# Kernel optimization log

Measured on AMD Instinct MI355X. Metric: run time of the kernel, lower is better.

## Reference

```python
import jax, jax.numpy as jnp
import numpy as np

N_VERT = 40962  # icosphere level-6 vertex count
K = 7           # 1-ring neighborhood size (self + 6 neighbors)


def setup_inputs() -> dict:
    key = jax.random.key(0)
    k1, k2, k3 = jax.random.split(key, 3)
    x = jax.random.normal(k1, (16, 256, N_VERT), dtype=jnp.float32)
    neigh_orders = jax.random.randint(k2, (N_VERT * K,), 0, N_VERT, dtype=jnp.int32)
    W = jax.random.normal(k3, (1, 2 * K), dtype=jnp.float32) * 0.1  # Linear(14 -> 1) weight
    b = jnp.zeros((1,), dtype=jnp.float32)
    return {"x": x, "neigh_orders": neigh_orders, "W": W, "b": b}


def reference(x, neigh_orders, W, b):
    # x: [B, C, N] features on spherical mesh vertices
    avg = jnp.mean(x, axis=1, keepdims=True)          # [B, 1, N] (AdaptiveAvgPool2d((1,None)))
    mx = jnp.max(x, axis=1, keepdims=True)            # [B, 1, N] (AdaptiveMaxPool2d((1,None)))
    pool = jnp.concatenate([avg, mx], axis=1)         # [B, 2, N]
    p = jnp.transpose(pool, (0, 2, 1))                # [B, N, 2]
    idx = neigh_orders.reshape(N_VERT, K)             # [N, 7] 1-ring neighbor indices
    g = p[:, idx, :]                                  # [B, N, 7, 2] neighbor gather
    g = g.reshape(p.shape[0], N_VERT, 2 * K)          # [B, N, 14]
    out = jnp.einsum('bnf,of->bno', g, W) + b         # [B, N, 1] Linear(14 -> 1)
    att = jax.nn.sigmoid(out)
    return jnp.transpose(att, (0, 2, 1))              # [B, 1, N] spatial attention map
```

## Files before the change

### kernel.cpp

```cpp
#include <hip/hip_runtime.h>
#include <math.h>

#define B_DIM 16
#define C_DIM 256
#define NV    40962
#define K_NEI 7
#define GRP   10240
#define MAIN_BLOCKS 2560

typedef float v2f __attribute__((ext_vector_type(2)));

__global__ __launch_bounds__(64) void pool_kernel(const float* __restrict__ x,
                                                  float4* __restrict__ pool) {
    if (blockIdx.x < MAIN_BLOCKS) {
        int t  = blockIdx.x * 64 + threadIdx.x;
        int b  = t / GRP;
        int r  = t - b * GRP;
        int n0 = 4 * r;

        const float* xb = x + (size_t)b * C_DIM * NV + n0;

        float s0 = 0.f, s1 = 0.f, s2 = 0.f, s3 = 0.f;
        float m0 = -INFINITY, m1 = -INFINITY, m2 = -INFINITY, m3 = -INFINITY;
        #pragma unroll 16
        for (int c = 0; c < C_DIM; ++c) {
            const float* p = xb + (size_t)c * NV;
            v2f va = __builtin_nontemporal_load(reinterpret_cast<const v2f*>(p));
            v2f vb = __builtin_nontemporal_load(reinterpret_cast<const v2f*>(p + 2));
            s0 += va.x; s1 += va.y; s2 += vb.x; s3 += vb.y;
            m0 = fmaxf(m0, va.x); m1 = fmaxf(m1, va.y);
            m2 = fmaxf(m2, vb.x); m3 = fmaxf(m3, vb.y);
        }
        const float inv = 1.0f / (float)C_DIM;
        size_t f4 = ((size_t)b * NV + n0) >> 1;
        pool[f4]     = make_float4(s0 * inv, m0, s1 * inv, m1);
        pool[f4 + 1] = make_float4(s2 * inv, m2, s3 * inv, m3);
    } else {
        __shared__ float2 part[64];
        int tid  = threadIdx.x;
        int col  = tid >> 1;
        int half = tid & 1;
        int b    = col >> 1;
        int n    = 40960 + (col & 1);

        const float* xb = x + (size_t)b * C_DIM * NV + n;
        float s = 0.f, m = -INFINITY;
        #pragma unroll 8
        for (int c = half * 128; c < half * 128 + 128; ++c) {
            float v = xb[(size_t)c * NV];
            s += v; m = fmaxf(m, v);
        }
        part[tid] = make_float2(s, m);
        __syncthreads();
        if (half == 0) {
            float2 a = part[tid], bb2 = part[tid + 1];
            float2* poolf2 = reinterpret_cast<float2*>(pool);
            poolf2[(size_t)b * NV + n] =
                make_float2((a.x + bb2.x) * (1.0f / (float)C_DIM), fmaxf(a.y, bb2.y));
        }
    }
}

__global__ void transpose_kernel(const float2* __restrict__ pool,
                                 float2* __restrict__ poolT) {
    __shared__ float2 tile[64][17];
    int n0 = blockIdx.x * 64;
    int i  = threadIdx.x & 63;
    int bq = threadIdx.x >> 6;
    #pragma unroll
    for (int p = 0; p < 4; ++p) {
        int b = p * 4 + bq;
        if (n0 + i < NV)
            tile[i][b] = pool[(size_t)b * NV + n0 + i];
    }
    __syncthreads();
    int valid = NV - n0; if (valid > 64) valid = 64;
    int nf4 = valid * 8;
    float4* dst = reinterpret_cast<float4*>(poolT + (size_t)n0 * 16);
    for (int e = threadIdx.x; e < nf4; e += 256) {
        int e2 = e * 2;
        int n  = e2 >> 4;
        int b  = e2 & 15;
        float2 a0 = tile[n][b];
        float2 a1 = tile[n][b + 1];
        dst[e] = make_float4(a0.x, a0.y, a1.x, a1.y);
    }
}

__global__ void att4_kernel(const float2* __restrict__ poolT,
                            const int* __restrict__ idx,
                            const float* __restrict__ W,
                            const float* __restrict__ bias,
                            float* __restrict__ out) {
    int tid = threadIdx.x;
    int n   = blockIdx.x * 64 + (tid >> 2);
    int bq  = tid & 3;
    if (n >= NV) return;

    float w[2 * K_NEI];
    #pragma unroll
    for (int i = 0; i < 2 * K_NEI; ++i) w[i] = W[i];
    float bb = bias[0];

    float acc[4];
    #pragma unroll
    for (int r = 0; r < 4; ++r) acc[r] = bb;

    #pragma unroll
    for (int k = 0; k < K_NEI; ++k) {
        int j = idx[n * K_NEI + k];
        const float4* L = reinterpret_cast<const float4*>(poolT + (size_t)j * 16 + bq * 4);
        float4 v0 = L[0];
        float4 v1 = L[1];
        acc[0] = fmaf(w[2 * k + 1], v0.y, fmaf(w[2 * k], v0.x, acc[0]));
        acc[1] = fmaf(w[2 * k + 1], v0.w, fmaf(w[2 * k], v0.z, acc[1]));
        acc[2] = fmaf(w[2 * k + 1], v1.y, fmaf(w[2 * k], v1.x, acc[2]));
        acc[3] = fmaf(w[2 * k + 1], v1.w, fmaf(w[2 * k], v1.z, acc[3]));
    }
    #pragma unroll
    for (int r = 0; r < 4; ++r)
        out[(size_t)(bq * 4 + r) * NV + n] = 1.0f / (1.0f + expf(-acc[r]));
}

extern "C" void kernel_launch(void* const* d_in, const int* in_sizes, int n_in,
                              void* d_out, int out_size, void* d_ws, size_t ws_size,
                              hipStream_t stream) {
    const float* x     = (const float*)d_in[0];
    const int*   neigh = (const int*)  d_in[1];
    const float* W     = (const float*)d_in[2];
    const float* bias  = (const float*)d_in[3];
    float*       out   = (float*)d_out;

    const size_t POOL_BYTES = (size_t)B_DIM * NV * sizeof(float2);

    float4* pool4 = (float4*)d_ws;
    float2* poolT = (float2*)((char*)d_ws + POOL_BYTES);

    pool_kernel<<<MAIN_BLOCKS + 1, 64, 0, stream>>>(x, pool4);

    int ntile = (NV + 63) / 64;
    transpose_kernel<<<ntile, 256, 0, stream>>>((const float2*)d_ws, poolT);
    att4_kernel<<<ntile, 256, 0, stream>>>(poolT, neigh, W, bias, out);
}
```

Measured before the change: 131.3 us.

## Use 16-byte aligned loads in pool kernel via odd-channel offset and LDS neighbor exchange

Because NV is odd, odd channel rows are only 8-byte aligned, so the old code issued two 8-byte loads per row. The new pool kernel loads even channels at n0 and odd channels at n0-2, both 16-byte aligned, and takes the missing odd-channel columns from the neighbouring thread through shared memory. The last thread in each block issues an extra 8-byte load. Blocks grow from 64 to 256 threads to support the exchange, which adds a barrier, LDS traffic and more registers per thread.

```diff
diff --git a/kernel.cpp b/kernel.cpp
--- a/kernel.cpp
+++ b/kernel.cpp
@@ -6,54 +6,94 @@
 #define NV    40962
 #define K_NEI 7
 #define GRP   10240
-#define MAIN_BLOCKS 2560
+#define NBLK_MAIN 640
 
 typedef float v2f __attribute__((ext_vector_type(2)));
+typedef float v4f __attribute__((ext_vector_type(4)));
 
-__global__ __launch_bounds__(64) void pool_kernel(const float* __restrict__ x,
-                                                  float4* __restrict__ pool) {
-    if (blockIdx.x < MAIN_BLOCKS) {
-        int t  = blockIdx.x * 64 + threadIdx.x;
+__global__ __launch_bounds__(256) void pool_kernel(const float* __restrict__ x,
+                                                   float4* __restrict__ pool) {
+    if (blockIdx.x < NBLK_MAIN) {
+        int t  = blockIdx.x * 256 + threadIdx.x;
         int b  = t / GRP;
         int r  = t - b * GRP;
         int n0 = 4 * r;
 
         const float* xb = x + (size_t)b * C_DIM * NV + n0;
+        bool last = (threadIdx.x == 255);
 
-        float s0 = 0.f, s1 = 0.f, s2 = 0.f, s3 = 0.f;
-        float m0 = -INFINITY, m1 = -INFINITY, m2 = -INFINITY, m3 = -INFINITY;
-        #pragma unroll 16
-        for (int c = 0; c < C_DIM; ++c) {
-            const float* p = xb + (size_t)c * NV;
-            v2f va = __builtin_nontemporal_load(reinterpret_cast<const v2f*>(p));
-            v2f vb = __builtin_nontemporal_load(reinterpret_cast<const v2f*>(p + 2));
-            s0 += va.x; s1 += va.y; s2 += vb.x; s3 += vb.y;
-            m0 = fmaxf(m0, va.x); m1 = fmaxf(m1, va.y);
-            m2 = fmaxf(m2, vb.x); m3 = fmaxf(m3, vb.y);
+        float sE0 = 0.f, sE1 = 0.f, sE2 = 0.f, sE3 = 0.f;
+        float mE0 = -INFINITY, mE1 = -INFINITY, mE2 = -INFINITY, mE3 = -INFINITY;
+        float sO0 = 0.f, sO1 = 0.f, sO2 = 0.f, sO3 = 0.f;
+        float mO0 = -INFINITY, mO1 = -INFINITY, mO2 = -INFINITY, mO3 = -INFINITY;
+        float sx2 = 0.f, sx3 = 0.f;
+        float mx2 = -INFINITY, mx3 = -INFINITY;
+
+        #pragma unroll 8
+        for (int cp = 0; cp < C_DIM / 2; ++cp) {
+            const float* pe = xb + (size_t)(2 * cp) * NV;
+            const float* po = xb + (size_t)(2 * cp + 1) * NV - 2;
+            v4f ve = __builtin_nontemporal_load(reinterpret_cast<const v4f*>(pe));
+            v4f vo = __builtin_nontemporal_load(reinterpret_cast<const v4f*>(po));
+            sE0 += ve.x; sE1 += ve.y; sE2 += ve.z; sE3 += ve.w;
+            mE0 = fmaxf(mE0, ve.x); mE1 = fmaxf(mE1, ve.y);
+            mE2 = fmaxf(mE2, ve.z); mE3 = fmaxf(mE3, ve.w);
+            sO0 += vo.x; sO1 += vo.y; sO2 += vo.z; sO3 += vo.w;
+            mO0 = fmaxf(mO0, vo.x); mO1 = fmaxf(mO1, vo.y);
+            mO2 = fmaxf(mO2, vo.z); mO3 = fmaxf(mO3, vo.w);
+            if (last) {
+                v2f v = __builtin_nontemporal_load(
+                            reinterpret_cast<const v2f*>(po + 4));
+                sx2 += v.x; sx3 += v.y;
+                mx2 = fmaxf(mx2, v.x); mx3 = fmaxf(mx3, v.y);
+            }
         }
+
+        __shared__ float4 shS[256];
+        __shared__ float4 shM[256];
+        shS[threadIdx.x] = make_float4(sO0, sO1, 0.f, 0.f);
+        shM[threadIdx.x] = make_float4(mO0, mO1, 0.f, 0.f);
+        __syncthreads();
+        float ns2, ns3, nm2, nm3;
+        if (!last) {
+            float4 a = shS[threadIdx.x + 1];
+            float4 c = shM[threadIdx.x + 1];
+            ns2 = a.x; ns3 = a.y; nm2 = c.x; nm3 = c.y;
+        } else {
+            ns2 = sx2; ns3 = sx3; nm2 = mx2; nm3 = mx3;
+        }
+
         const float inv = 1.0f / (float)C_DIM;
+        float s0 = sE0 + sO2, s1 = sE1 + sO3, s2 = sE2 + ns2, s3 = sE3 + ns3;
+        float m0 = fmaxf(mE0, mO2), m1 = fmaxf(mE1, mO3);
+        float m2 = fmaxf(mE2, nm2), m3 = fmaxf(mE3, nm3);
+
         size_t f4 = ((size_t)b * NV + n0) >> 1;
         pool[f4]     = make_float4(s0 * inv, m0, s1 * inv, m1);
         pool[f4 + 1] = make_float4(s2 * inv, m2, s3 * inv, m3);
     } else {
         __shared__ float2 part[64];
-        int tid  = threadIdx.x;
-        int col  = tid >> 1;
-        int half = tid & 1;
-        int b    = col >> 1;
-        int n    = 40960 + (col & 1);
-
-        const float* xb = x + (size_t)b * C_DIM * NV + n;
-        float s = 0.f, m = -INFINITY;
-        #pragma unroll 8
-        for (int c = half * 128; c < half * 128 + 128; ++c) {
-            float v = xb[(size_t)c * NV];
-            s += v; m = fmaxf(m, v);
+        int tid = threadIdx.x;
+        if (tid < 64) {
+            int col  = tid >> 1;
+            int half = tid & 1;
+            int b    = col >> 1;
+            int n    = 40960 + (col & 1);
+            const float* xb = x + (size_t)b * C_DIM * NV + n;
+            float s = 0.f, m = -INFINITY;
+            #pragma unroll 8
+            for (int c = half * 128; c < half * 128 + 128; ++c) {
+                float v = xb[(size_t)c * NV];
+                s += v; m = fmaxf(m, v);
+            }
+            part[tid] = make_float2(s, m);
         }
-        part[tid] = make_float2(s, m);
         __syncthreads();
-        if (half == 0) {
+        if (tid < 64 && (tid & 1) == 0) {
             float2 a = part[tid], bb2 = part[tid + 1];
+            int col = tid >> 1;
+            int b   = col >> 1;
+            int n   = 40960 + (col & 1);
             float2* poolf2 = reinterpret_cast<float2*>(pool);
             poolf2[(size_t)b * NV + n] =
                 make_float2((a.x + bb2.x) * (1.0f / (float)C_DIM), fmaxf(a.y, bb2.y));
@@ -136,7 +176,7 @@
     float4* pool4 = (float4*)d_ws;
     float2* poolT = (float2*)((char*)d_ws + POOL_BYTES);
 
-    pool_kernel<<<MAIN_BLOCKS + 1, 64, 0, stream>>>(x, pool4);
+    pool_kernel<<<NBLK_MAIN + 1, 256, 0, stream>>>(x, pool4);
 
     int ntile = (NV + 63) / 64;
     transpose_kernel<<<ntile, 256, 0, stream>>>((const float2*)d_ws, poolT);
```

New measurement: 167.2 us. +27.4%, slower.
